# Optimization experiments

Hardware: AMD Instinct MI355X
Metric: run time of the kernel (lower is better)

## Reference

```python
import jax, jax.numpy as jnp
import numpy as np

DIM = 96
HEADS = 3
WIN = 7
HID = 384  # dim * mlp_ratio
EPS = 1e-5


def layernorm(x, w, b):
    mu = jnp.mean(x, axis=-1, keepdims=True)
    var = jnp.mean((x - mu) ** 2, axis=-1, keepdims=True)
    return (x - mu) * jax.lax.rsqrt(var + EPS) * w + b


def setup_inputs() -> dict:
    key = jax.random.key(0)
    ks = jax.random.split(key, 8)
    s = lambda n: 1.0 / np.sqrt(n)
    return {
        "x": jax.random.normal(ks[0], (8, DIM, 224, 224), dtype=jnp.float32),
        "norm1_w": jnp.ones((DIM,), jnp.float32),
        "norm1_b": jnp.zeros((DIM,), jnp.float32),
        "qkv_w": jax.random.normal(ks[1], (DIM, 3 * DIM), jnp.float32) * s(DIM),
        "qkv_b": jnp.zeros((3 * DIM,), jnp.float32),
        "proj_w": jax.random.normal(ks[2], (DIM, DIM), jnp.float32) * s(DIM),
        "proj_b": jnp.zeros((DIM,), jnp.float32),
        "norm2_w": jnp.ones((DIM,), jnp.float32),
        "norm2_b": jnp.zeros((DIM,), jnp.float32),
        "fc1_w": jax.random.normal(ks[3], (DIM, HID), jnp.float32) * s(DIM),
        "fc1_b": jnp.zeros((HID,), jnp.float32),
        "fc2_w": jax.random.normal(ks[4], (HID, DIM), jnp.float32) * s(HID),
        "fc2_b": jnp.zeros((DIM,), jnp.float32),
    }


def swin_block(x, norm1_w, norm1_b, qkv_w, qkv_b, proj_w, proj_b,
               norm2_w, norm2_b, fc1_w, fc1_b, fc2_w, fc2_b):
    B, C, H, W = x.shape
    hd = C // HEADS
    scale = hd ** -0.5
    N = WIN * WIN
    # [B, H*W, C]
    tok = jnp.transpose(x.reshape(B, C, H * W), (0, 2, 1))
    shortcut = tok
    t = layernorm(tok, norm1_w, norm1_b).reshape(B, H, W, C)
    nH, nW = H // WIN, W // WIN
    wins = t.reshape(B, nH, WIN, nW, WIN, C).transpose(0, 1, 3, 2, 4, 5)
    wins = wins.reshape(-1, N, C)  # [B*nH*nW, N, C]
    # window MHA
    qkv = (wins @ qkv_w + qkv_b).reshape(-1, N, 3, HEADS, hd)
    q, k, v = jnp.moveaxis(qkv, 2, 0)  # each [Bw, N, HEADS, hd]
    attn = jnp.einsum('bnhd,bmhd->bhnm', q, k) * scale
    attn = jax.nn.softmax(attn, axis=-1)
    o = jnp.einsum('bhnm,bmhd->bnhd', attn, v).reshape(-1, N, C)
    o = o @ proj_w + proj_b
    # window reverse
    o = o.reshape(B, nH, nW, WIN, WIN, C).transpose(0, 1, 3, 2, 4, 5)
    o = o.reshape(B, H * W, C)
    t = shortcut + o
    # MLP block
    m = layernorm(t, norm2_w, norm2_b)
    m = jax.nn.gelu(m @ fc1_w + fc1_b, approximate=False) @ fc2_w + fc2_b
    t = t + m
    return jnp.transpose(t, (0, 2, 1)).reshape(B, C, H, W)


def reference(x, norm1_w, norm1_b, qkv_w, qkv_b, proj_w, proj_b,
              norm2_w, norm2_b, fc1_w, fc1_b, fc2_w, fc2_b):
    return swin_block(x, norm1_w, norm1_b, qkv_w, qkv_b, proj_w, proj_b,
                      norm2_w, norm2_b, fc1_w, fc1_b, fc2_w, fc2_b)
```

## Files before the change

### kernel.cpp

```cpp
#include <hip/hip_runtime.h>


typedef __bf16 bf16;
typedef __attribute__((ext_vector_type(8))) __bf16 bf16x8;
typedef __attribute__((ext_vector_type(4))) float f32x4;
typedef __attribute__((ext_vector_type(4))) int i32x4;

#define LDA 104
#define LDV 72
#define LDW 233
#define TOKW 6144

union U8 { int i[4]; bf16x8 v; };

__device__ __forceinline__ f32x4 mfma16(bf16x8 a, bf16x8 b, f32x4 c) {
    return __builtin_amdgcn_mfma_f32_16x16x32_bf16(a, b, c, 0, 0, 0);
}
__device__ __forceinline__ int pkbf(float lo, float hi) {
    int r; asm("v_cvt_pk_bf16_f32 %0, %1, %2" : "=v"(r) : "v"(lo), "v"(hi)); return r;
}
__device__ __forceinline__ float rcpf(float x) {
    float r; asm("v_rcp_f32 %0, %1" : "=v"(r) : "v"(x)); return r;
}
__device__ __forceinline__ float gelu_f(float v) {
    const float a = -2.30220770f, b = -0.10294852f;
    float e = exp2f(v * __builtin_fmaf(b, v * v, a));
    return v * rcpf(1.f + e);
}

__global__ void swin_wprep(const float* __restrict__ qkv_w,
                           const float* __restrict__ proj_w,
                           const float* __restrict__ fc1_w,
                           const float* __restrict__ fc2_w,
                           bf16* __restrict__ wsT) {
    int i = blockIdx.x * 256 + threadIdx.x;
    if (i < 27648) { int n = i / 96, k = i - n * 96; wsT[i] = (bf16)qkv_w[k * 288 + n]; }
    else if (i < 36864) { int j = i - 27648, n = j / 96, k = j - n * 96; wsT[i] = (bf16)proj_w[k * 96 + n]; }
    else if (i < 73728) { int j = i - 36864, n = j / 96, k = j - n * 96; wsT[i] = (bf16)fc1_w[k * 384 + n]; }
    else if (i < 110592){ int j = i - 73728, n = j / 384, k = j - n * 384; wsT[i] = (bf16)fc2_w[k * 96 + n]; }
}

__global__ void swin_padfill(bf16* __restrict__ tokW) {
    int id = blockIdx.x * 256 + threadIdx.x;
    int win = id / 180, r = id - win * 180;
    int row = 49 + r / 12, c8 = r - (r / 12) * 12;
    *(i32x4*)(tokW + (size_t)win * TOKW + row * 96 + c8 * 8) = i32x4{0, 0, 0, 0};
}

__global__ __launch_bounds__(256)
void swin_gather(const float* __restrict__ x, bf16* __restrict__ tokW) {
    __shared__ bf16 sT[96 * LDW];
    const int tid = threadIdx.x;
    const int bi = blockIdx.x;
    const int b = bi / 224, h = bi - b * 224;
    const int wy = h / 7, ty = h - wy * 7;
    const size_t xbase = (size_t)b * 4816896 + (size_t)h * 224;

#pragma unroll
    for (int i = 0; i < 21; ++i) {
        int id = i * 256 + tid;
        int c = id / 56, w4 = id - c * 56;
        f32x4 v = *(const f32x4*)(x + xbase + (size_t)c * 50176 + w4 * 4);
#pragma unroll
        for (int j = 0; j < 4; ++j) sT[c * LDW + w4 * 4 + j] = (bf16)v[j];
    }
    __syncthreads();

#pragma unroll
    for (int i = 0; i < 11; ++i) {
        int id = i * 256 + tid;
        if (id < 2688) {
            int win = id / 84, r = id - win * 84;
            int tx = r / 12, c8 = r - tx * 12;
            bf16x8 v;
#pragma unroll
            for (int j = 0; j < 8; ++j) v[j] = sT[(c8 * 8 + j) * LDW + win * 7 + tx];
            *(i32x4*)(tokW + (size_t)(b * 1024 + wy * 32 + win) * TOKW
                      + (ty * 7 + tx) * 96 + c8 * 8) = *(i32x4*)&v;
        }
    }
}

__global__ __launch_bounds__(256)
void swin_scatter(const bf16* __restrict__ tokW, float* __restrict__ out) {
    __shared__ bf16 sT[96 * LDW];
    const int tid = threadIdx.x;
    const int bi = blockIdx.x;
    const int b = bi / 224, h = bi - b * 224;
    const int wy = h / 7, ty = h - wy * 7;
    const size_t obase = (size_t)b * 4816896 + (size_t)h * 224;

#pragma unroll
    for (int i = 0; i < 11; ++i) {
        int id = i * 256 + tid;
        if (id < 2688) {
            int win = id / 84, r = id - win * 84;
            int tx = r / 12, c8 = r - tx * 12;
            bf16x8 v = *(const bf16x8*)(tokW + (size_t)(b * 1024 + wy * 32 + win) * TOKW
                                        + (ty * 7 + tx) * 96 + c8 * 8);
#pragma unroll
            for (int j = 0; j < 8; ++j) sT[(c8 * 8 + j) * LDW + win * 7 + tx] = v[j];
        }
    }
    __syncthreads();

#pragma unroll
    for (int i = 0; i < 21; ++i) {
        int id = i * 256 + tid;
        int c = id / 56, w4 = id - c * 56;
        f32x4 v;
#pragma unroll
        for (int j = 0; j < 4; ++j) v[j] = (float)sT[c * LDW + w4 * 4 + j];
        *(f32x4*)(out + obase + (size_t)c * 50176 + w4 * 4) = v;
    }
}

__device__ __forceinline__ bf16x8 bload(const bf16* T, const float* worig,
                                        int nrow, int k0, int K, int N, bool wok) {
    if (wok) return *(const bf16x8*)(T + (size_t)nrow * K + k0);
    bf16x8 f;
#pragma unroll
    for (int j = 0; j < 8; ++j) f[j] = (bf16)worig[(size_t)(k0 + j) * N + nrow];
    return f;
}

__global__ __launch_bounds__(256, 4)
void swin_fused(const float* __restrict__ x, bf16* __restrict__ tokW,
                const float* __restrict__ n1w, const float* __restrict__ n1b,
                const float* __restrict__ qkvw, const float* __restrict__ qkvb,
                const float* __restrict__ projw, const float* __restrict__ projb,
                const float* __restrict__ n2w, const float* __restrict__ n2b,
                const float* __restrict__ fc1w, const float* __restrict__ fc1b,
                const float* __restrict__ fc2w, const float* __restrict__ fc2b,
                const bf16* __restrict__ wsT,
                float* __restrict__ out, int fast_i, int wok_i) {
    __shared__ __attribute__((aligned(16))) bf16 L[20224];
    bf16* RB = L;
    bf16* RC = L + 6656;
    bf16* RV = L + 13312;

    const bool fast = fast_i != 0;
    const bool wok  = wok_i != 0;

    const int tid  = threadIdx.x;
    const int wave = tid >> 6;
    const int lane = tid & 63;
    const int g    = lane >> 4;
    const int q16  = lane & 15;

    const int win = blockIdx.x;
    const int b  = win >> 10;
    const int wy = (win >> 5) & 31;
    const int wx = win & 31;
    const int h0 = wy * 7, w0 = wx * 7;
    const size_t xbase = (size_t)b * 4816896;
    const bf16* myWin = tokW + (size_t)win * TOKW;

    if (fast) {
#pragma unroll
        for (int i = 0; i < 3; ++i) {
            int id = i * 256 + tid;
            int row = id / 12, c8 = id - row * 12;
            *(i32x4*)&RB[row * LDA + c8 * 8] = *(const i32x4*)(myWin + row * 96 + c8 * 8);
        }
    } else {
        for (int i = 0; i < 24; ++i) {
            int id = i * 256 + tid;
            if (id < 4704) {
                int c = id / 49, pix = id - c * 49;
                int ty = pix / 7, tx = pix - ty * 7;
                RB[pix * LDA + c] =
                    (bf16)x[xbase + (size_t)c * 50176 + (h0 + ty) * 224 + w0 + tx];
            } else if (id < 6144) {
                int j = id - 4704;
                int row = 49 + j / 96, c = j - (j / 96) * 96;
                RB[row * LDA + c] = (bf16)0.f;
            }
        }
    }
    __syncthreads();

    {
        int r = tid >> 2, p = tid & 3;
        const int c0 = p * 24;
        bf16* rp = &RB[r * LDA + c0];
        bf16x8 v0 = *(const bf16x8*)rp;
        bf16x8 v1 = *(const bf16x8*)(rp + 8);
        bf16x8 v2 = *(const bf16x8*)(rp + 16);
        float s = 0.f, s2 = 0.f;
#pragma unroll
        for (int j = 0; j < 8; ++j) {
            float a = (float)v0[j], c = (float)v1[j], d = (float)v2[j];
            s += a + c + d; s2 += a * a + c * c + d * d;
        }
        s += __shfl_xor(s, 1);  s2 += __shfl_xor(s2, 1);
        s += __shfl_xor(s, 2);  s2 += __shfl_xor(s2, 2);
        float mu = s * (1.f / 96.f);
        float rs = rsqrtf(fmaxf(s2 * (1.f / 96.f) - mu * mu, 0.f) + 1e-5f);
        bf16x8 o0, o1, o2;
#pragma unroll
        for (int j = 0; j < 8; ++j) {
            o0[j] = (bf16)(((float)v0[j] - mu) * rs * n1w[c0 + j] + n1b[c0 + j]);
            o1[j] = (bf16)(((float)v1[j] - mu) * rs * n1w[c0 + 8 + j] + n1b[c0 + 8 + j]);
            o2[j] = (bf16)(((float)v2[j] - mu) * rs * n1w[c0 + 16 + j] + n1b[c0 + 16 + j]);
        }
        *(bf16x8*)rp = o0; *(bf16x8*)(rp + 8) = o1; *(bf16x8*)(rp + 16) = o2;
    }
    __syncthreads();

    bf16x8 afrag[3][4];
#pragma unroll
    for (int s = 0; s < 3; ++s)
#pragma unroll
        for (int m = 0; m < 4; ++m)
            afrag[s][m] = *(const bf16x8*)&RB[(m * 16 + q16) * LDA + s * 32 + g * 8];
    __syncthreads();

    const bf16* qkvT  = wsT;
    const bf16* projT = wsT + 27648;
    const bf16* fc1T  = wsT + 36864;
    const bf16* fc2T  = wsT + 73728;

    for (int nt = wave; nt < 18; nt += 4) {
        const int nrow = nt * 16 + q16;
        f32x4 acc[4] = {{0,0,0,0},{0,0,0,0},{0,0,0,0},{0,0,0,0}};
#pragma unroll
        for (int s = 0; s < 3; ++s) {
            bf16x8 bf = bload(qkvT, qkvw, nrow, s * 32 + g * 8, 96, 288, wok);
#pragma unroll
            for (int m = 0; m < 4; ++m) acc[m] = mfma16(afrag[s][m], bf, acc[m]);
        }
        float bias = qkvb[nrow];
#pragma unroll
        for (int m = 0; m < 4; ++m)
#pragma unroll
            for (int r = 0; r < 4; ++r) {
                float v = acc[m][r] + bias;
                int row = m * 16 + g * 4 + r;
                bf16 hv = (bf16)v;
                if (nrow < 96)        RB[row * LDA + nrow] = hv;
                else if (nrow < 192)  RC[row * LDA + (nrow - 96)] = hv;
                else                  RV[(nrow - 192) * LDV + row] = hv;
            }
    }
    __syncthreads();

    const float sc_l2e = 0.17677669529663688f * 1.4426950408889634f;
    const bool hi5 = (lane & 32) != 0;
    const int addr0 = ((lane & 16) << 3) | (q16 << 2);
    const int addr1 = addr0 + 64;
    f32x4 oacc[3][2];
#pragma unroll
    for (int h = 0; h < 3; ++h) {
        bf16x8 bq = *(const bf16x8*)&RB[(wave * 16 + q16) * LDA + h * 32 + g * 8];
        f32x4 s4s[4];
#pragma unroll
        for (int kt = 0; kt < 4; ++kt) {
            bf16x8 ak = *(const bf16x8*)&RC[(kt * 16 + q16) * LDA + h * 32 + g * 8];
            f32x4 z = {0, 0, 0, 0};
            s4s[kt] = mfma16(ak, bq, z);
        }
        float m0 = -1e30f;
#pragma unroll
        for (int kt = 0; kt < 3; ++kt)
#pragma unroll
            for (int r = 0; r < 4; ++r) m0 = fmaxf(m0, s4s[kt][r]);
        m0 = fmaxf(m0, (g == 0) ? s4s[3][0] : -1e30f);
        m0 = fmaxf(m0, __shfl_xor(m0, 16));
        m0 = fmaxf(m0, __shfl_xor(m0, 32));
        float ss = 0.f;
#pragma unroll
        for (int kt = 0; kt < 3; ++kt)
#pragma unroll
            for (int r = 0; r < 4; ++r) {
                float e = exp2f((s4s[kt][r] - m0) * sc_l2e);
                s4s[kt][r] = e; ss += e;
            }
        {
            float e = (g == 0) ? exp2f((s4s[3][0] - m0) * sc_l2e) : 0.f;
            s4s[3][0] = e; ss += e;
            s4s[3][1] = 0.f; s4s[3][2] = 0.f; s4s[3][3] = 0.f;
        }
        ss += __shfl_xor(ss, 16);
        ss += __shfl_xor(ss, 32);
        float inv = rcpf(ss);

        int u[4][2];
#pragma unroll
        for (int kt = 0; kt < 4; ++kt) {
            u[kt][0] = pkbf(s4s[kt][0], s4s[kt][1]);
            u[kt][1] = pkbf(s4s[kt][2], s4s[kt][3]);
        }
        bf16x8 ap[2];
#pragma unroll
        for (int kh = 0; kh < 2; ++kh) {
            U8 w;
            int a0 = __builtin_amdgcn_ds_bpermute(addr0, u[kh * 2][0]);
            int b0 = __builtin_amdgcn_ds_bpermute(addr0, u[kh * 2 + 1][0]);
            w.i[0] = hi5 ? b0 : a0;
            int a1 = __builtin_amdgcn_ds_bpermute(addr0, u[kh * 2][1]);
            int b1 = __builtin_amdgcn_ds_bpermute(addr0, u[kh * 2 + 1][1]);
            w.i[1] = hi5 ? b1 : a1;
            int a2 = __builtin_amdgcn_ds_bpermute(addr1, u[kh * 2][0]);
            int b2 = __builtin_amdgcn_ds_bpermute(addr1, u[kh * 2 + 1][0]);
            w.i[2] = hi5 ? b2 : a2;
            int a3 = __builtin_amdgcn_ds_bpermute(addr1, u[kh * 2][1]);
            int b3 = __builtin_amdgcn_ds_bpermute(addr1, u[kh * 2 + 1][1]);
            w.i[3] = hi5 ? b3 : a3;
            ap[kh] = w.v;
        }
#pragma unroll
        for (int n2 = 0; n2 < 2; ++n2) {
            int d0 = (h * 32 + n2 * 16 + q16) * LDV;
            f32x4 oa = {0, 0, 0, 0};
            oa = mfma16(*(const bf16x8*)&RV[d0 + g * 8], ap[0], oa);
            oa = mfma16(*(const bf16x8*)&RV[d0 + 32 + g * 8], ap[1], oa);
#pragma unroll
            for (int r = 0; r < 4; ++r) oa[r] *= inv;
            oacc[h][n2] = oa;
        }
    }
    __syncthreads();

    {
        int u2[3][2][2];
#pragma unroll
        for (int h = 0; h < 3; ++h)
#pragma unroll
            for (int n2 = 0; n2 < 2; ++n2) {
                u2[h][n2][0] = pkbf(oacc[h][n2][0], oacc[h][n2][1]);
                u2[h][n2][1] = pkbf(oacc[h][n2][2], oacc[h][n2][3]);
            }
        bf16x8 aoM[3];
#pragma unroll
        for (int s = 0; s < 3; ++s) {
            U8 w;
            int a0 = __builtin_amdgcn_ds_bpermute(addr0, u2[s][0][0]);
            int b0 = __builtin_amdgcn_ds_bpermute(addr0, u2[s][1][0]);
            w.i[0] = hi5 ? b0 : a0;
            int a1 = __builtin_amdgcn_ds_bpermute(addr0, u2[s][0][1]);
            int b1 = __builtin_amdgcn_ds_bpermute(addr0, u2[s][1][1]);
            w.i[1] = hi5 ? b1 : a1;
            int a2 = __builtin_amdgcn_ds_bpermute(addr1, u2[s][0][0]);
            int b2 = __builtin_amdgcn_ds_bpermute(addr1, u2[s][1][0]);
            w.i[2] = hi5 ? b2 : a2;
            int a3 = __builtin_amdgcn_ds_bpermute(addr1, u2[s][0][1]);
            int b3 = __builtin_amdgcn_ds_bpermute(addr1, u2[s][1][1]);
            w.i[3] = hi5 ? b3 : a3;
            aoM[s] = w.v;
        }
#pragma unroll
        for (int nt = 0; nt < 6; ++nt) {
            int nrow = nt * 16 + q16;
            f32x4 pacc = {0, 0, 0, 0};
#pragma unroll
            for (int s = 0; s < 3; ++s) {
                bf16x8 bf = bload(projT, projw, nrow, s * 32 + g * 8, 96, 96, wok);
                pacc = mfma16(aoM[s], bf, pacc);
            }
            float bias = projb[nrow];
#pragma unroll
            for (int r = 0; r < 4; ++r) {
                int row = wave * 16 + g * 4 + r;
                float sc;
                if (fast) sc = (float)myWin[row * 96 + nrow];
                else      sc = (row < 49)
                    ? x[xbase + (size_t)nrow * 50176 + (h0 + row / 7) * 224 + w0 + row % 7]
                    : 0.f;
                RV[row * LDA + nrow] = (bf16)(pacc[r] + bias + sc);
            }
        }
    }
    __syncthreads();

    {
        int r = tid >> 2, p = tid & 3;
        const int c0 = p * 24;
        const bf16* rp = &RV[r * LDA + c0];
        bf16x8 v0 = *(const bf16x8*)rp;
        bf16x8 v1 = *(const bf16x8*)(rp + 8);
        bf16x8 v2 = *(const bf16x8*)(rp + 16);
        float s = 0.f, s2 = 0.f;
#pragma unroll
        for (int j = 0; j < 8; ++j) {
            float a = (float)v0[j], c = (float)v1[j], d = (float)v2[j];
            s += a + c + d; s2 += a * a + c * c + d * d;
        }
        s += __shfl_xor(s, 1);  s2 += __shfl_xor(s2, 1);
        s += __shfl_xor(s, 2);  s2 += __shfl_xor(s2, 2);
        float mu = s * (1.f / 96.f);
        float rs = rsqrtf(fmaxf(s2 * (1.f / 96.f) - mu * mu, 0.f) + 1e-5f);
        bf16x8 o0, o1, o2;
#pragma unroll
        for (int j = 0; j < 8; ++j) {
            o0[j] = (bf16)(((float)v0[j] - mu) * rs * n2w[c0 + j] + n2b[c0 + j]);
            o1[j] = (bf16)(((float)v1[j] - mu) * rs * n2w[c0 + 8 + j] + n2b[c0 + 8 + j]);
            o2[j] = (bf16)(((float)v2[j] - mu) * rs * n2w[c0 + 16 + j] + n2b[c0 + 16 + j]);
        }
        bf16* wp = &RB[r * LDA + c0];
        *(bf16x8*)wp = o0; *(bf16x8*)(wp + 8) = o1; *(bf16x8*)(wp + 16) = o2;
    }
    __syncthreads();

    const int npt = (wave < 2) ? 2 : 1;
    f32x4 f2acc[2][4] = {{{0,0,0,0},{0,0,0,0},{0,0,0,0},{0,0,0,0}},
                         {{0,0,0,0},{0,0,0,0},{0,0,0,0},{0,0,0,0}}};
    for (int ch = 0; ch < 4; ++ch) {
#pragma unroll
        for (int t = 0; t < 2; ++t) {
            if (t < npt) {
                int ntl = (t == 0) ? wave : wave + 4;
                int nrow = (ch * 6 + ntl) * 16 + q16;
                f32x4 acc[4] = {{0,0,0,0},{0,0,0,0},{0,0,0,0},{0,0,0,0}};
#pragma unroll
                for (int s = 0; s < 3; ++s) {
                    bf16x8 bf = bload(fc1T, fc1w, nrow, s * 32 + g * 8, 96, 384, wok);
#pragma unroll
                    for (int m = 0; m < 4; ++m) {
                        bf16x8 a = *(const bf16x8*)&RB[(m * 16 + q16) * LDA + s * 32 + g * 8];
                        acc[m] = mfma16(a, bf, acc[m]);
                    }
                }
                float bias = fc1b[nrow];
#pragma unroll
                for (int m = 0; m < 4; ++m)
#pragma unroll
                    for (int r = 0; r < 4; ++r)
                        RC[(m * 16 + g * 4 + r) * LDA + ntl * 16 + q16] =
                            (bf16)gelu_f(acc[m][r] + bias);
            }
        }
        __syncthreads();
#pragma unroll
        for (int s = 0; s < 3; ++s) {
            bf16x8 a0 = *(const bf16x8*)&RC[(q16)      * LDA + s * 32 + g * 8];
            bf16x8 a1 = *(const bf16x8*)&RC[(16 + q16) * LDA + s * 32 + g * 8];
            bf16x8 a2 = *(const bf16x8*)&RC[(32 + q16) * LDA + s * 32 + g * 8];
            bf16x8 a3 = *(const bf16x8*)&RC[(48 + q16) * LDA + s * 32 + g * 8];
#pragma unroll
            for (int t = 0; t < 2; ++t) {
                if (t < npt) {
                    int nt = (t == 0) ? wave : wave + 4;
                    int nrow = nt * 16 + q16;
                    bf16x8 bf = bload(fc2T, fc2w, nrow, ch * 96 + s * 32 + g * 8, 384, 96, wok);
                    f2acc[t][0] = mfma16(a0, bf, f2acc[t][0]);
                    f2acc[t][1] = mfma16(a1, bf, f2acc[t][1]);
                    f2acc[t][2] = mfma16(a2, bf, f2acc[t][2]);
                    f2acc[t][3] = mfma16(a3, bf, f2acc[t][3]);
                }
            }
        }
        __syncthreads();
    }

#pragma unroll
    for (int t = 0; t < 2; ++t) {
        if (t < npt) {
            int col = ((t == 0) ? wave : wave + 4) * 16 + q16;
            float bias = fc2b[col];
#pragma unroll
            for (int m = 0; m < 4; ++m)
#pragma unroll
                for (int r = 0; r < 4; ++r) {
                    int row = m * 16 + g * 4 + r;
                    float t2 = (float)RV[row * LDA + col];
                    RV[row * LDA + col] = (bf16)(f2acc[t][m][r] + bias + t2);
                }
        }
    }
    __syncthreads();

    if (fast) {
#pragma unroll
        for (int i = 0; i < 3; ++i) {
            int id = i * 256 + tid;
            if (id < 588) {
                int row = id / 12, c8 = id - row * 12;
                *(i32x4*)(tokW + (size_t)win * TOKW + row * 96 + c8 * 8) =
                    *(const i32x4*)&RV[row * LDA + c8 * 8];
            }
        }
    } else {
        for (int i = 0; i < 19; ++i) {
            int id = i * 256 + tid;
            if (id < 4704) {
                int c = id / 49, pix = id - c * 49;
                int ty = pix / 7, tx = pix - ty * 7;
                out[xbase + (size_t)c * 50176 + (h0 + ty) * 224 + w0 + tx] =
                    (float)RV[pix * LDA + c];
            }
        }
    }
}

extern "C" void kernel_launch(void* const* d_in, const int* in_sizes, int n_in,
                              void* d_out, int out_size, void* d_ws, size_t ws_size,
                              hipStream_t stream) {
    const float* x      = (const float*)d_in[0];
    const float* n1w    = (const float*)d_in[1];
    const float* n1b    = (const float*)d_in[2];
    const float* qkv_w  = (const float*)d_in[3];
    const float* qkv_b  = (const float*)d_in[4];
    const float* proj_w = (const float*)d_in[5];
    const float* proj_b = (const float*)d_in[6];
    const float* n2w    = (const float*)d_in[7];
    const float* n2b    = (const float*)d_in[8];
    const float* fc1_w  = (const float*)d_in[9];
    const float* fc1_b  = (const float*)d_in[10];
    const float* fc2_w  = (const float*)d_in[11];
    const float* fc2_b  = (const float*)d_in[12];
    float* out = (float*)d_out;

    const size_t TOKW_OFF = 225280;
    const int wok  = (ws_size >= 221184) ? 1 : 0;
    const int fast = (ws_size >= TOKW_OFF + 100663296ull) ? 1 : 0;
    bf16* wsT  = (bf16*)d_ws;
    bf16* tokW = (bf16*)((char*)d_ws + TOKW_OFF);

    if (wok)
        swin_wprep<<<dim3(432), dim3(256), 0, stream>>>(qkv_w, proj_w, fc1_w, fc2_w, wsT);
    if (fast) {
        swin_padfill<<<dim3(5760), dim3(256), 0, stream>>>(tokW);
        swin_gather<<<dim3(1792), dim3(256), 0, stream>>>(x, tokW);
    }
    swin_fused<<<dim3(8192), dim3(256), 0, stream>>>(
        x, tokW, n1w, n1b, qkv_w, qkv_b, proj_w, proj_b, n2w, n2b,
        fc1_w, fc1_b, fc2_w, fc2_b, wsT, out, fast, wok);
    if (fast)
        swin_scatter<<<dim3(1792), dim3(256), 0, stream>>>(tokW, out);
}
```

Baseline: 444.5 us.

## Add specialized fused window kernel for fast path with register-resident fragments

Adds a new fused kernel used when the workspace holds both prepped bf16 weights and the gathered token buffer. It drops the runtime fast/wok branches and the fallback loads of the original fp32 weights. The Q projection is kept in registers via lane permutes instead of being stored to LDS. LDS shrinks by dropping one region, and the residual is read straight from the token buffer in bf16. The result is written back in place into the token buffer as bf16, which risks extra rounding and adds complexity in exchange for fewer LDS round trips and higher occupancy.

```diff
diff --git a/kernel.cpp b/kernel.cpp
--- a/kernel.cpp
+++ b/kernel.cpp
@@ -3,8 +3,10 @@
 
 typedef __bf16 bf16;
 typedef __attribute__((ext_vector_type(8))) __bf16 bf16x8;
+typedef __attribute__((ext_vector_type(4))) __bf16 bf16x4;
 typedef __attribute__((ext_vector_type(4))) float f32x4;
 typedef __attribute__((ext_vector_type(4))) int i32x4;
+typedef __attribute__((ext_vector_type(2))) int i32x2;
 
 #define LDA 104
 #define LDV 72
@@ -26,6 +28,29 @@
     const float a = -2.30220770f, b = -0.10294852f;
     float e = exp2f(v * __builtin_fmaf(b, v * v, a));
     return v * rcpf(1.f + e);
+}
+__device__ __forceinline__ float bf2f(int dw, int hi) {
+    union { int i; float f; } u;
+    u.i = hi ? (dw & 0xffff0000) : (dw << 16);
+    return u.f;
+}
+
+__device__ __forceinline__ bf16x8 xp(int p0, int p1, int q0, int q1,
+                                     int addr0, int addr1, bool hi5) {
+    U8 w;
+    int a0 = __builtin_amdgcn_ds_bpermute(addr0, p0);
+    int b0 = __builtin_amdgcn_ds_bpermute(addr0, q0);
+    w.i[0] = hi5 ? b0 : a0;
+    int a1 = __builtin_amdgcn_ds_bpermute(addr0, p1);
+    int b1 = __builtin_amdgcn_ds_bpermute(addr0, q1);
+    w.i[1] = hi5 ? b1 : a1;
+    int a2 = __builtin_amdgcn_ds_bpermute(addr1, p0);
+    int b2 = __builtin_amdgcn_ds_bpermute(addr1, q0);
+    w.i[2] = hi5 ? b2 : a2;
+    int a3 = __builtin_amdgcn_ds_bpermute(addr1, p1);
+    int b3 = __builtin_amdgcn_ds_bpermute(addr1, q1);
+    w.i[3] = hi5 ? b3 : a3;
+    return w.v;
 }
 
 __global__ void swin_wprep(const float* __restrict__ qkv_w,
@@ -115,6 +140,301 @@
     }
 }
 
+__global__ __launch_bounds__(256, 4)
+void swin_fused_fast(bf16* __restrict__ tokW,
+                     const float* __restrict__ n1w, const float* __restrict__ n1b,
+                     const float* __restrict__ qkvb, const float* __restrict__ projb,
+                     const float* __restrict__ n2w, const float* __restrict__ n2b,
+                     const float* __restrict__ fc1b, const float* __restrict__ fc2b,
+                     const bf16* __restrict__ wsT) {
+    __shared__ __attribute__((aligned(16))) bf16 L[13568];
+    bf16* RB = L;
+    bf16* RV = L + 6656;
+
+    const int tid  = threadIdx.x;
+    const int wave = tid >> 6;
+    const int lane = tid & 63;
+    const int g    = lane >> 4;
+    const int q16  = lane & 15;
+
+    const int win = blockIdx.x;
+    bf16* myWin = tokW + (size_t)win * TOKW;
+
+    const bool hi5 = (lane & 32) != 0;
+    const int addr0 = ((lane & 16) << 3) | (q16 << 2);
+    const int addr1 = addr0 + 64;
+
+    const bf16* qkvT  = wsT;
+    const bf16* projT = wsT + 27648;
+    const bf16* fc1T  = wsT + 36864;
+    const bf16* fc2T  = wsT + 73728;
+
+#pragma unroll
+    for (int i = 0; i < 3; ++i) {
+        int id = i * 256 + tid;
+        int row = id / 12, c8 = id - row * 12;
+        *(i32x4*)&RB[row * LDA + c8 * 8] = *(const i32x4*)(myWin + row * 96 + c8 * 8);
+    }
+    __syncthreads();
+
+    {
+        int r = tid >> 2, p = tid & 3;
+        const int c0 = p * 24;
+        bf16* rp = &RB[r * LDA + c0];
+        bf16x8 v0 = *(const bf16x8*)rp;
+        bf16x8 v1 = *(const bf16x8*)(rp + 8);
+        bf16x8 v2 = *(const bf16x8*)(rp + 16);
+        float s = 0.f, s2 = 0.f;
+#pragma unroll
+        for (int j = 0; j < 8; ++j) {
+            float a = (float)v0[j], c = (float)v1[j], d = (float)v2[j];
+            s += a + c + d; s2 += a * a + c * c + d * d;
+        }
+        s += __shfl_xor(s, 1);  s2 += __shfl_xor(s2, 1);
+        s += __shfl_xor(s, 2);  s2 += __shfl_xor(s2, 2);
+        float mu = s * (1.f / 96.f);
+        float rs = rsqrtf(fmaxf(s2 * (1.f / 96.f) - mu * mu, 0.f) + 1e-5f);
+        bf16x8 o0, o1, o2;
+#pragma unroll
+        for (int j = 0; j < 8; ++j) {
+            o0[j] = (bf16)(((float)v0[j] - mu) * rs * n1w[c0 + j] + n1b[c0 + j]);
+            o1[j] = (bf16)(((float)v1[j] - mu) * rs * n1w[c0 + 8 + j] + n1b[c0 + 8 + j]);
+            o2[j] = (bf16)(((float)v2[j] - mu) * rs * n1w[c0 + 16 + j] + n1b[c0 + 16 + j]);
+        }
+        *(bf16x8*)rp = o0; *(bf16x8*)(rp + 8) = o1; *(bf16x8*)(rp + 16) = o2;
+    }
+    __syncthreads();
+
+    bf16x8 afrag[3][4];
+#pragma unroll
+    for (int s = 0; s < 3; ++s)
+#pragma unroll
+        for (int tt = 0; tt < 4; ++tt)
+            afrag[s][tt] = *(const bf16x8*)&RB[(tt * 16 + q16) * LDA + s * 32 + g * 8];
+    __syncthreads();
+
+    bf16x8 bq[3];
+    {
+        int uq[6][2];
+#pragma unroll
+        for (int nt = 0; nt < 6; ++nt) {
+            f32x4 qa = {0, 0, 0, 0};
+#pragma unroll
+            for (int s = 0; s < 3; ++s)
+                qa = mfma16(*(const bf16x8*)(qkvT + (nt * 16 + q16) * 96 + s * 32 + g * 8),
+                            afrag[s][wave], qa);
+            f32x4 qb = *(const f32x4*)(qkvb + nt * 16 + g * 4);
+            uq[nt][0] = pkbf(qa[0] + qb[0], qa[1] + qb[1]);
+            uq[nt][1] = pkbf(qa[2] + qb[2], qa[3] + qb[3]);
+        }
+#pragma unroll
+        for (int h = 0; h < 3; ++h)
+            bq[h] = xp(uq[2 * h][0], uq[2 * h][1], uq[2 * h + 1][0], uq[2 * h + 1][1],
+                       addr0, addr1, hi5);
+    }
+
+#pragma unroll 1
+    for (int i = 0; i < 3; ++i) {
+        const int nt = 6 + wave + i * 4;
+        const int nrow = nt * 16 + q16;
+        f32x4 acc[4] = {{0,0,0,0},{0,0,0,0},{0,0,0,0},{0,0,0,0}};
+#pragma unroll
+        for (int s = 0; s < 3; ++s) {
+            bf16x8 bf = *(const bf16x8*)(qkvT + nrow * 96 + s * 32 + g * 8);
+#pragma unroll
+            for (int m = 0; m < 4; ++m) acc[m] = mfma16(afrag[s][m], bf, acc[m]);
+        }
+        float bias = qkvb[nrow];
+        if (nt < 12) {
+#pragma unroll
+            for (int m = 0; m < 4; ++m)
+#pragma unroll
+                for (int r = 0; r < 4; ++r)
+                    RB[(m * 16 + g * 4 + r) * LDA + (nt - 6) * 16 + q16] =
+                        (bf16)(acc[m][r] + bias);
+        } else {
+#pragma unroll
+            for (int m = 0; m < 4; ++m)
+#pragma unroll
+                for (int r = 0; r < 4; ++r)
+                    RV[((nt - 12) * 16 + q16) * LDV + m * 16 + g * 4 + r] =
+                        (bf16)(acc[m][r] + bias);
+        }
+    }
+    __syncthreads();
+
+    const float sc_l2e = 0.17677669529663688f * 1.4426950408889634f;
+    f32x4 oacc[3][2];
+#pragma unroll
+    for (int h = 0; h < 3; ++h) {
+        f32x4 s4s[4];
+#pragma unroll
+        for (int kt = 0; kt < 4; ++kt) {
+            bf16x8 ak = *(const bf16x8*)&RB[(kt * 16 + q16) * LDA + h * 32 + g * 8];
+            f32x4 z = {0, 0, 0, 0};
+            s4s[kt] = mfma16(ak, bq[h], z);
+        }
+        float m0 = -1e30f;
+#pragma unroll
+        for (int kt = 0; kt < 3; ++kt)
+#pragma unroll
+            for (int r = 0; r < 4; ++r) m0 = fmaxf(m0, s4s[kt][r]);
+        m0 = fmaxf(m0, (g == 0) ? s4s[3][0] : -1e30f);
+        m0 = fmaxf(m0, __shfl_xor(m0, 16));
+        m0 = fmaxf(m0, __shfl_xor(m0, 32));
+        float ss = 0.f;
+#pragma unroll
+        for (int kt = 0; kt < 3; ++kt)
+#pragma unroll
+            for (int r = 0; r < 4; ++r) {
+                float e = exp2f((s4s[kt][r] - m0) * sc_l2e);
+                s4s[kt][r] = e; ss += e;
+            }
+        {
+            float e = (g == 0) ? exp2f((s4s[3][0] - m0) * sc_l2e) : 0.f;
+            s4s[3][0] = e; ss += e;
+            s4s[3][1] = 0.f; s4s[3][2] = 0.f; s4s[3][3] = 0.f;
+        }
+        ss += __shfl_xor(ss, 16);
+        ss += __shfl_xor(ss, 32);
+        float inv = rcpf(ss);
+
+        int u[4][2];
+#pragma unroll
+        for (int kt = 0; kt < 4; ++kt) {
+            u[kt][0] = pkbf(s4s[kt][0], s4s[kt][1]);
+            u[kt][1] = pkbf(s4s[kt][2], s4s[kt][3]);
+        }
+        bf16x8 ap0 = xp(u[0][0], u[0][1], u[1][0], u[1][1], addr0, addr1, hi5);
+        bf16x8 ap1 = xp(u[2][0], u[2][1], u[3][0], u[3][1], addr0, addr1, hi5);
+#pragma unroll
+        for (int n2 = 0; n2 < 2; ++n2) {
+            int d0 = (h * 32 + n2 * 16 + q16) * LDV;
+            f32x4 oa = {0, 0, 0, 0};
+            oa = mfma16(*(const bf16x8*)&RV[d0 + g * 8], ap0, oa);
+            oa = mfma16(*(const bf16x8*)&RV[d0 + 32 + g * 8], ap1, oa);
+#pragma unroll
+            for (int r = 0; r < 4; ++r) oa[r] *= inv;
+            oacc[h][n2] = oa;
+        }
+    }
+    __syncthreads();
+
+    bf16x8 bt2n[3];
+    {
+        int uo[3][2][2];
+#pragma unroll
+        for (int h = 0; h < 3; ++h)
+#pragma unroll
+            for (int n2 = 0; n2 < 2; ++n2) {
+                uo[h][n2][0] = pkbf(oacc[h][n2][0], oacc[h][n2][1]);
+                uo[h][n2][1] = pkbf(oacc[h][n2][2], oacc[h][n2][3]);
+            }
+        bf16x8 aoM[3];
+#pragma unroll
+        for (int s = 0; s < 3; ++s)
+            aoM[s] = xp(uo[s][0][0], uo[s][0][1], uo[s][1][0], uo[s][1][1],
+                        addr0, addr1, hi5);
+        const int tok = wave * 16 + q16;
+        float t2f[6][4];
+#pragma unroll
+        for (int nt = 0; nt < 6; ++nt) {
+            f32x4 pa = {0, 0, 0, 0};
+#pragma unroll
+            for (int s = 0; s < 3; ++s)
+                pa = mfma16(*(const bf16x8*)(projT + (nt * 16 + q16) * 96 + s * 32 + g * 8),
+                            aoM[s], pa);
+            f32x4 pb = *(const f32x4*)(projb + nt * 16 + g * 4);
+            bf16x4 rv = *(const bf16x4*)(myWin + tok * 96 + nt * 16 + g * 4);
+#pragma unroll
+            for (int r = 0; r < 4; ++r) t2f[nt][r] = pa[r] + pb[r] + (float)rv[r];
+        }
+        float s = 0.f, s2 = 0.f;
+#pragma unroll
+        for (int nt = 0; nt < 6; ++nt)
+#pragma unroll
+            for (int r = 0; r < 4; ++r) { float v = t2f[nt][r]; s += v; s2 += v * v; }
+        s += __shfl_xor(s, 16);  s2 += __shfl_xor(s2, 16);
+        s += __shfl_xor(s, 32);  s2 += __shfl_xor(s2, 32);
+        float mu = s * (1.f / 96.f);
+        float rs = rsqrtf(fmaxf(s2 * (1.f / 96.f) - mu * mu, 0.f) + 1e-5f);
+        int u3[6][2];
+#pragma unroll
+        for (int nt = 0; nt < 6; ++nt) {
+            f32x4 nw = *(const f32x4*)(n2w + nt * 16 + g * 4);
+            f32x4 nb = *(const f32x4*)(n2b + nt * 16 + g * 4);
+            float tn0 = (t2f[nt][0] - mu) * rs * nw[0] + nb[0];
+            float tn1 = (t2f[nt][1] - mu) * rs * nw[1] + nb[1];
+            float tn2 = (t2f[nt][2] - mu) * rs * nw[2] + nb[2];
+            float tn3 = (t2f[nt][3] - mu) * rs * nw[3] + nb[3];
+            u3[nt][0] = pkbf(tn0, tn1);
+            u3[nt][1] = pkbf(tn2, tn3);
+            i32x2 pr = {pkbf(t2f[nt][0], t2f[nt][1]), pkbf(t2f[nt][2], t2f[nt][3])};
+            *(i32x2*)&RV[tok * LDA + nt * 16 + g * 4] = pr;
+        }
+#pragma unroll
+        for (int s5 = 0; s5 < 3; ++s5)
+            bt2n[s5] = xp(u3[2 * s5][0], u3[2 * s5][1], u3[2 * s5 + 1][0], u3[2 * s5 + 1][1],
+                          addr0, addr1, hi5);
+    }
+
+    f32x4 facc[6] = {{0,0,0,0},{0,0,0,0},{0,0,0,0},{0,0,0,0},{0,0,0,0},{0,0,0,0}};
+#pragma unroll 1
+    for (int ch = 0; ch < 6; ++ch) {
+        int u4[4][2];
+#pragma unroll
+        for (int t4 = 0; t4 < 4; ++t4) {
+            f32x4 ha = {0, 0, 0, 0};
+#pragma unroll
+            for (int s = 0; s < 3; ++s)
+                ha = mfma16(*(const bf16x8*)(fc1T + (ch * 64 + t4 * 16 + q16) * 96
+                                             + s * 32 + g * 8),
+                            bt2n[s], ha);
+            f32x4 hb = *(const f32x4*)(fc1b + ch * 64 + t4 * 16 + g * 4);
+            float hg0 = gelu_f(ha[0] + hb[0]);
+            float hg1 = gelu_f(ha[1] + hb[1]);
+            float hg2 = gelu_f(ha[2] + hb[2]);
+            float hg3 = gelu_f(ha[3] + hb[3]);
+            u4[t4][0] = pkbf(hg0, hg1);
+            u4[t4][1] = pkbf(hg2, hg3);
+        }
+        bf16x8 bh0 = xp(u4[0][0], u4[0][1], u4[1][0], u4[1][1], addr0, addr1, hi5);
+        bf16x8 bh1 = xp(u4[2][0], u4[2][1], u4[3][0], u4[3][1], addr0, addr1, hi5);
+#pragma unroll
+        for (int nt = 0; nt < 6; ++nt) {
+            facc[nt] = mfma16(*(const bf16x8*)(fc2T + (nt * 16 + q16) * 384
+                                               + ch * 64 + g * 8), bh0, facc[nt]);
+            facc[nt] = mfma16(*(const bf16x8*)(fc2T + (nt * 16 + q16) * 384
+                                               + ch * 64 + 32 + g * 8), bh1, facc[nt]);
+        }
+    }
+
+    {
+        const int tok = wave * 16 + q16;
+#pragma unroll
+        for (int nt = 0; nt < 6; ++nt) {
+            f32x4 fb = *(const f32x4*)(fc2b + nt * 16 + g * 4);
+            i32x2 t2p = *(const i32x2*)&RV[tok * LDA + nt * 16 + g * 4];
+            float v0 = facc[nt][0] + fb[0] + bf2f(t2p[0], 0);
+            float v1 = facc[nt][1] + fb[1] + bf2f(t2p[0], 1);
+            float v2 = facc[nt][2] + fb[2] + bf2f(t2p[1], 0);
+            float v3 = facc[nt][3] + fb[3] + bf2f(t2p[1], 1);
+            i32x2 po = {pkbf(v0, v1), pkbf(v2, v3)};
+            *(i32x2*)&RB[tok * LDA + nt * 16 + g * 4] = po;
+        }
+    }
+    __syncthreads();
+
+#pragma unroll
+    for (int i = 0; i < 3; ++i) {
+        int id = i * 256 + tid;
+        if (id < 588) {
+            int row = id / 12, c8 = id - row * 12;
+            *(i32x4*)(myWin + row * 96 + c8 * 8) = *(const i32x4*)&RB[row * LDA + c8 * 8];
+        }
+    }
+}
+
 __device__ __forceinline__ bf16x8 bload(const bf16* T, const float* worig,
                                         int nrow, int k0, int K, int N, bool wok) {
     if (wok) return *(const bf16x8*)(T + (size_t)nrow * K + k0);
@@ -125,7 +445,7 @@
 }
 
 __global__ __launch_bounds__(256, 4)
-void swin_fused(const float* __restrict__ x, bf16* __restrict__ tokW,
+void swin_fused_safe(const float* __restrict__ x, bf16* __restrict__ tokW,
                 const float* __restrict__ n1w, const float* __restrict__ n1b,
                 const float* __restrict__ qkvw, const float* __restrict__ qkvb,
                 const float* __restrict__ projw, const float* __restrict__ projb,
@@ -252,13 +572,13 @@
     f32x4 oacc[3][2];
 #pragma unroll
     for (int h = 0; h < 3; ++h) {
-        bf16x8 bq = *(const bf16x8*)&RB[(wave * 16 + q16) * LDA + h * 32 + g * 8];
+        bf16x8 bqv = *(const bf16x8*)&RB[(wave * 16 + q16) * LDA + h * 32 + g * 8];
         f32x4 s4s[4];
 #pragma unroll
         for (int kt = 0; kt < 4; ++kt) {
             bf16x8 ak = *(const bf16x8*)&RC[(kt * 16 + q16) * LDA + h * 32 + g * 8];
             f32x4 z = {0, 0, 0, 0};
-            s4s[kt] = mfma16(ak, bq, z);
+            s4s[kt] = mfma16(ak, bqv, z);
         }
         float m0 = -1e30f;
 #pragma unroll
@@ -291,30 +611,14 @@
             u[kt][0] = pkbf(s4s[kt][0], s4s[kt][1]);
             u[kt][1] = pkbf(s4s[kt][2], s4s[kt][3]);
         }
-        bf16x8 ap[2];
-#pragma unroll
-        for (int kh = 0; kh < 2; ++kh) {
-            U8 w;
-            int a0 = __builtin_amdgcn_ds_bpermute(addr0, u[kh * 2][0]);
-            int b0 = __builtin_amdgcn_ds_bpermute(addr0, u[kh * 2 + 1][0]);
-            w.i[0] = hi5 ? b0 : a0;
-            int a1 = __builtin_amdgcn_ds_bpermute(addr0, u[kh * 2][1]);
-            int b1 = __builtin_amdgcn_ds_bpermute(addr0, u[kh * 2 + 1][1]);
-            w.i[1] = hi5 ? b1 : a1;
-            int a2 = __builtin_amdgcn_ds_bpermute(addr1, u[kh * 2][0]);
-            int b2 = __builtin_amdgcn_ds_bpermute(addr1, u[kh * 2 + 1][0]);
-            w.i[2] = hi5 ? b2 : a2;
-            int a3 = __builtin_amdgcn_ds_bpermute(addr1, u[kh * 2][1]);
-            int b3 = __builtin_amdgcn_ds_bpermute(addr1, u[kh * 2 + 1][1]);
-            w.i[3] = hi5 ? b3 : a3;
-            ap[kh] = w.v;
-        }
+        bf16x8 ap0 = xp(u[0][0], u[0][1], u[1][0], u[1][1], addr0, addr1, hi5);
+        bf16x8 ap1 = xp(u[2][0], u[2][1], u[3][0], u[3][1], addr0, addr1, hi5);
 #pragma unroll
         for (int n2 = 0; n2 < 2; ++n2) {
             int d0 = (h * 32 + n2 * 16 + q16) * LDV;
             f32x4 oa = {0, 0, 0, 0};
-            oa = mfma16(*(const bf16x8*)&RV[d0 + g * 8], ap[0], oa);
-            oa = mfma16(*(const bf16x8*)&RV[d0 + 32 + g * 8], ap[1], oa);
+            oa = mfma16(*(const bf16x8*)&RV[d0 + g * 8], ap0, oa);
+            oa = mfma16(*(const bf16x8*)&RV[d0 + 32 + g * 8], ap1, oa);
 #pragma unroll
             for (int r = 0; r < 4; ++r) oa[r] *= inv;
             oacc[h][n2] = oa;
@@ -333,22 +637,9 @@
             }
         bf16x8 aoM[3];
 #pragma unroll
-        for (int s = 0; s < 3; ++s) {
-            U8 w;
-            int a0 = __builtin_amdgcn_ds_bpermute(addr0, u2[s][0][0]);
-            int b0 = __builtin_amdgcn_ds_bpermute(addr0, u2[s][1][0]);
-            w.i[0] = hi5 ? b0 : a0;
-            int a1 = __builtin_amdgcn_ds_bpermute(addr0, u2[s][0][1]);
-            int b1 = __builtin_amdgcn_ds_bpermute(addr0, u2[s][1][1]);
-            w.i[1] = hi5 ? b1 : a1;
-            int a2 = __builtin_amdgcn_ds_bpermute(addr1, u2[s][0][0]);
-            int b2 = __builtin_amdgcn_ds_bpermute(addr1, u2[s][1][0]);
-            w.i[2] = hi5 ? b2 : a2;
-            int a3 = __builtin_amdgcn_ds_bpermute(addr1, u2[s][0][1]);
-            int b3 = __builtin_amdgcn_ds_bpermute(addr1, u2[s][1][1]);
-            w.i[3] = hi5 ? b3 : a3;
-            aoM[s] = w.v;
-        }
+        for (int s = 0; s < 3; ++s)
+            aoM[s] = xp(u2[s][0][0], u2[s][0][1], u2[s][1][0], u2[s][1][1],
+                        addr0, addr1, hi5);
 #pragma unroll
         for (int nt = 0; nt < 6; ++nt) {
             int nrow = nt * 16 + q16;
@@ -523,9 +814,14 @@
         swin_padfill<<<dim3(5760), dim3(256), 0, stream>>>(tokW);
         swin_gather<<<dim3(1792), dim3(256), 0, stream>>>(x, tokW);
     }
-    swin_fused<<<dim3(8192), dim3(256), 0, stream>>>(
-        x, tokW, n1w, n1b, qkv_w, qkv_b, proj_w, proj_b, n2w, n2b,
-        fc1_w, fc1_b, fc2_w, fc2_b, wsT, out, fast, wok);
+    if (fast && wok) {
+        swin_fused_fast<<<dim3(8192), dim3(256), 0, stream>>>(
+            tokW, n1w, n1b, qkv_b, proj_b, n2w, n2b, fc1_b, fc2_b, wsT);
+    } else {
+        swin_fused_safe<<<dim3(8192), dim3(256), 0, stream>>>(
+            x, tokW, n1w, n1b, qkv_w, qkv_b, proj_w, proj_b, n2w, n2b,
+            fc1_w, fc1_b, fc2_w, fc2_b, wsT, out, fast, wok);
+    }
     if (fast)
         swin_scatter<<<dim3(1792), dim3(256), 0, stream>>>(tokW, out);
 }
```

Measured after the change: 711.3 us. 60.0% more time.
